# Performance work log

Measured on AMD Instinct MI355X. Metric: run time of the kernel, lower is better.

The kernel has to match this reference:

```python
import jax, jax.numpy as jnp
import numpy as np

N_NODES = 100000
N_EDGES = 1600000
N_GRAPHS = 64
IN_F = 128
H_F = 128
N_CLS = 10


def setup_inputs() -> dict:
    key = jax.random.key(0)
    ks = jax.random.split(key, 10)
    feat = jax.random.normal(ks[0], (N_NODES, IN_F), dtype=jnp.float32)
    W1 = jax.random.normal(ks[1], (IN_F, H_F), dtype=jnp.float32) * 0.05
    b1 = jax.random.normal(ks[2], (H_F,), dtype=jnp.float32) * 0.05
    W2 = jax.random.normal(ks[3], (H_F, H_F), dtype=jnp.float32) * 0.05
    b2 = jax.random.normal(ks[4], (H_F,), dtype=jnp.float32) * 0.05
    Wp = jax.random.normal(ks[5], (H_F, N_CLS), dtype=jnp.float32) * 0.05
    bp = jax.random.normal(ks[6], (N_CLS,), dtype=jnp.float32) * 0.05
    src = jax.random.randint(ks[7], (N_EDGES,), 0, N_NODES, dtype=jnp.int32)
    dst = jax.random.randint(ks[8], (N_EDGES,), 0, N_NODES, dtype=jnp.int32)
    graph_id = jnp.sort(jax.random.randint(ks[9], (N_NODES,), 0, N_GRAPHS, dtype=jnp.int32))
    return {"feat": feat, "W1": W1, "b1": b1, "W2": W2, "b2": b2,
            "Wp": Wp, "bp": bp, "src": src, "dst": dst, "graph_id": graph_id}


def reference(feat, W1, b1, W2, b2, Wp, bp, src, dst, graph_id):
    # copy_u + sum: each dst node sums features of its source neighbors
    def agg(h):
        return jax.ops.segment_sum(h[src], dst, num_segments=N_NODES)

    h = jax.nn.relu(agg(feat) @ W1 + b1)   # conv1 + ReLU
    h = jax.nn.relu(agg(h) @ W2 + b2)      # conv2 + ReLU (num_messagepasses=2)

    # dgl.mean_nodes: per-graph mean pooling over nodes
    sums = jax.ops.segment_sum(h, graph_id, num_segments=N_GRAPHS)      # [G, H]
    cnts = jax.ops.segment_sum(jnp.ones((N_NODES, 1), h.dtype), graph_id,
                               num_segments=N_GRAPHS)                    # [G, 1]
    graph_feats = sums / jnp.maximum(cnts, 1.0)
    return graph_feats @ Wp + bp
```

## Files before the change

kernel.cpp:

```cpp
#include <hip/hip_runtime.h>

#define NF 128
#define NGRAPHS 64
#define NCLS 10
#define NPARTS 256
#define PART_SHIFT 9
#define PART_NODES 512
#define PART_CAP 9216
#define SPLIT_TILE 2048
#define AS_STRIDE 136
#define SRC_BITS 17

typedef __attribute__((ext_vector_type(8))) short bf16x8;
typedef __attribute__((ext_vector_type(4))) float f32x4;
typedef __attribute__((ext_vector_type(8))) unsigned short u16x8;

__device__ __forceinline__ float bf2f(unsigned short u) {
    union { unsigned int i; float f; } v; v.i = ((unsigned int)u) << 16; return v.f;
}
__device__ __forceinline__ unsigned short f2bf(float f) {
    union { float f; unsigned int i; } v; v.f = f;
    unsigned int lsb = (v.i >> 16) & 1;
    v.i += 0x7fffu + lsb;
    return (unsigned short)(v.i >> 16);
}

__device__ __forceinline__ void gather_node(
    const unsigned short* __restrict__ x, const int* __restrict__ offs,
    const int* __restrict__ eid, int node, int n, int c, float acc[8]) {
#pragma unroll
    for (int r = 0; r < 8; ++r) acc[r] = 0.f;
    if (node >= n) return;
    int j = offs[node];
    int end = offs[node + 1];
    for (; j + 8 <= end; j += 8) {
        int s0 = eid[j + 0], s1 = eid[j + 1], s2 = eid[j + 2], s3 = eid[j + 3];
        int s4 = eid[j + 4], s5 = eid[j + 5], s6 = eid[j + 6], s7 = eid[j + 7];
        u16x8 v0 = ((const u16x8*)(x + (size_t)s0 * NF))[c];
        u16x8 v1 = ((const u16x8*)(x + (size_t)s1 * NF))[c];
        u16x8 v2 = ((const u16x8*)(x + (size_t)s2 * NF))[c];
        u16x8 v3 = ((const u16x8*)(x + (size_t)s3 * NF))[c];
        u16x8 v4 = ((const u16x8*)(x + (size_t)s4 * NF))[c];
        u16x8 v5 = ((const u16x8*)(x + (size_t)s5 * NF))[c];
        u16x8 v6 = ((const u16x8*)(x + (size_t)s6 * NF))[c];
        u16x8 v7 = ((const u16x8*)(x + (size_t)s7 * NF))[c];
#pragma unroll
        for (int r = 0; r < 8; ++r)
            acc[r] += ((bf2f(v0[r]) + bf2f(v1[r])) + (bf2f(v2[r]) + bf2f(v3[r])))
                    + ((bf2f(v4[r]) + bf2f(v5[r])) + (bf2f(v6[r]) + bf2f(v7[r])));
    }
    if (j + 4 <= end) {
        int s0 = eid[j + 0], s1 = eid[j + 1], s2 = eid[j + 2], s3 = eid[j + 3];
        u16x8 v0 = ((const u16x8*)(x + (size_t)s0 * NF))[c];
        u16x8 v1 = ((const u16x8*)(x + (size_t)s1 * NF))[c];
        u16x8 v2 = ((const u16x8*)(x + (size_t)s2 * NF))[c];
        u16x8 v3 = ((const u16x8*)(x + (size_t)s3 * NF))[c];
#pragma unroll
        for (int r = 0; r < 8; ++r)
            acc[r] += (bf2f(v0[r]) + bf2f(v1[r])) + (bf2f(v2[r]) + bf2f(v3[r]));
        j += 4;
    }
    for (; j < end; ++j) {
        int s0 = eid[j];
        u16x8 v0 = ((const u16x8*)(x + (size_t)s0 * NF))[c];
#pragma unroll
        for (int r = 0; r < 8; ++r) acc[r] += bf2f(v0[r]);
    }
}

__global__ __launch_bounds__(256) void prep_kernel(
    const float* __restrict__ feat, unsigned short* __restrict__ featbf,
    const float* __restrict__ W1, const float* __restrict__ W2,
    unsigned short* __restrict__ Wt1, unsigned short* __restrict__ Wt2,
    float* __restrict__ sums, int* __restrict__ gcur, int nv4) {
    int gtid = blockIdx.x * 256 + threadIdx.x;
    int nthreads = gridDim.x * 256;
    for (int i = gtid; i < nv4; i += nthreads) {
        float4 v = ((const float4*)feat)[i];
        ushort4 o;
        o.x = f2bf(v.x); o.y = f2bf(v.y); o.z = f2bf(v.z); o.w = f2bf(v.w);
        ((ushort4*)featbf)[i] = o;
    }
    for (int i = gtid; i < 2 * NF * NF; i += nthreads) {
        const float* W = (i < NF * NF) ? W1 : W2;
        unsigned short* Wt = (i < NF * NF) ? Wt1 : Wt2;
        int id = i & (NF * NF - 1);
        int f = id >> 7;
        int k = id & 127;
        Wt[f * NF + k] = f2bf(W[k * NF + f]);
    }
    for (int i = gtid; i < NGRAPHS * NF; i += nthreads) sums[i] = 0.f;
    if (gtid < NPARTS) gcur[gtid] = 0;
}

__global__ __launch_bounds__(256) void split_kernel(
    const int* __restrict__ src, const int* __restrict__ dst,
    unsigned int* __restrict__ records, int* __restrict__ gcur, int ne) {
    __shared__ unsigned int stage[SPLIT_TILE];
    __shared__ int hcnt[NPARTS];
    __shared__ int hscan[NPARTS];
    __shared__ int hcur[NPARTS];
    __shared__ int hg[NPARTS];
    int t = threadIdx.x;

    int tile0 = blockIdx.x * SPLIT_TILE;
    int cnt = min(SPLIT_TILE, ne - tile0);
    if (cnt <= 0) return;
    hcnt[t] = 0;
    __syncthreads();
    int dv[SPLIT_TILE / 256], sv[SPLIT_TILE / 256];
#pragma unroll
    for (int k2 = 0; k2 < SPLIT_TILE / 256; ++k2) {
        int i = k2 * 256 + t;
        if (i < cnt) {
            dv[k2] = dst[tile0 + i];
            sv[k2] = src[tile0 + i];
            atomicAdd(&hcnt[dv[k2] >> PART_SHIFT], 1);
        }
    }
    __syncthreads();
    hscan[t] = hcnt[t];
    __syncthreads();
    for (int off = 1; off < NPARTS; off <<= 1) {
        int v = (t >= off) ? hscan[t - off] : 0;
        __syncthreads();
        hscan[t] += v;
        __syncthreads();
    }
    hcur[t] = hscan[t] - hcnt[t];
    hg[t] = hcnt[t] ? atomicAdd(&gcur[t], hcnt[t]) : 0;
    __syncthreads();
#pragma unroll
    for (int k2 = 0; k2 < SPLIT_TILE / 256; ++k2) {
        int i = k2 * 256 + t;
        if (i < cnt) {
            int d = dv[k2];
            int pos = atomicAdd(&hcur[d >> PART_SHIFT], 1);
            stage[pos] = (((unsigned int)(d & (PART_NODES - 1))) << SRC_BITS)
                         | (unsigned int)sv[k2];
        }
    }
    __syncthreads();
    int grp = t >> 4;
    int lt = t & 15;
    for (int p = grp; p < NPARTS; p += 16) {
        int c = hcnt[p];
        if (c == 0) continue;
        int b = hscan[p] - c;
        int g = hg[p];
        if (g + c > PART_CAP) c = max(0, PART_CAP - g);
        unsigned int* outp = records + (size_t)p * PART_CAP + g;
        for (int i = lt; i < c; i += 16) outp[i] = stage[b + i];
    }
}

__global__ __launch_bounds__(256) void build_kernel(
    const unsigned int* __restrict__ records, const int* __restrict__ gcur,
    int* __restrict__ offs, int* __restrict__ eid, int n) {
    __shared__ int deg[PART_NODES];
    __shared__ int ps[NPARTS];
    __shared__ int wsum[4];
    __shared__ unsigned int rc[PART_CAP];
    int t = threadIdx.x;
    int p = blockIdx.x;

    ps[t] = min(gcur[t], PART_CAP);
    __syncthreads();
    for (int off = 1; off < NPARTS; off <<= 1) {
        int v = (t >= off) ? ps[t - off] : 0;
        __syncthreads();
        ps[t] += v;
        __syncthreads();
    }
    int L = min(gcur[p], PART_CAP);
    int base_g = ps[p] - L;
    if (p == 0 && t == 0) offs[n] = ps[NPARTS - 1];

    int lo = p << PART_SHIFT;
    int nn = min(n - lo, PART_NODES);
    if (nn <= 0) return;

    deg[t] = 0;
    deg[t + 256] = 0;
    __syncthreads();

    const unsigned int* rp = records + (size_t)p * PART_CAP;
    for (int i = t; i < L; i += 256) {
        unsigned int r = rp[i];
        rc[i] = r;
        atomicAdd(&deg[r >> SRC_BITS], 1);
    }
    __syncthreads();

    int v0 = deg[2 * t];
    int v1 = deg[2 * t + 1];
    int tsum = v0 + v1;
    int lane = t & 63, w = t >> 6;
    int sc = tsum;
    for (int off = 1; off < 64; off <<= 1) {
        int u = __shfl_up(sc, off, 64);
        if (lane >= off) sc += u;
    }
    if (lane == 63) wsum[w] = sc;
    __syncthreads();
    if (t == 0) {
        int a = 0;
        for (int k = 0; k < 4; ++k) { int v = wsum[k]; wsum[k] = a; a += v; }
    }
    __syncthreads();
    int run = sc - tsum + wsum[w];
    deg[2 * t] = run;
    if (2 * t < nn) offs[lo + 2 * t] = base_g + run;
    run += v0;
    deg[2 * t + 1] = run;
    if (2 * t + 1 < nn) offs[lo + 2 * t + 1] = base_g + run;
    __syncthreads();

    for (int i = t; i < L; i += 256) {
        unsigned int r = rc[i];
        int pos = atomicAdd(&deg[r >> SRC_BITS], 1);
        eid[base_g + pos] = (int)(r & ((1u << SRC_BITS) - 1));
    }
}

__global__ __launch_bounds__(256) void gather_gemm1(
    const unsigned short* __restrict__ x, const int* __restrict__ offs,
    const int* __restrict__ eid, const unsigned short* __restrict__ Wt,
    const float* __restrict__ bias, unsigned short* __restrict__ out, int n) {
    __shared__ unsigned short As[16 * AS_STRIDE];
    int wave = threadIdx.x >> 6;
    int lane = threadIdx.x & 63;
    int q = lane >> 4;
    int c = lane & 15;
    int node_base = blockIdx.x * 16;
    int row = wave * 4 + q;

    float acc[8];
    gather_node(x, offs, eid, node_base + row, n, c, acc);
    {
        u16x8 o;
#pragma unroll
        for (int r = 0; r < 8; ++r) o[r] = f2bf(acc[r]);
        *(u16x8*)(&As[row * AS_STRIDE + c * 8]) = o;
    }
    __syncthreads();

    int m16 = c;
    int n0 = wave * 32;
    const unsigned short* b0r = Wt + (size_t)(n0 + m16) * NF + q * 8;
    const unsigned short* b1r = b0r + 16 * NF;
    f32x4 acc0 = {0.f, 0.f, 0.f, 0.f};
    f32x4 acc1 = {0.f, 0.f, 0.f, 0.f};
#pragma unroll
    for (int kk = 0; kk < 4; ++kk) {
        bf16x8 a  = *(const bf16x8*)(&As[m16 * AS_STRIDE + kk * 32 + q * 8]);
        bf16x8 b0 = *(const bf16x8*)(b0r + kk * 32);
        bf16x8 b1 = *(const bf16x8*)(b1r + kk * 32);
        acc0 = __builtin_amdgcn_mfma_f32_16x16x32_bf16(a, b0, acc0, 0, 0, 0);
        acc1 = __builtin_amdgcn_mfma_f32_16x16x32_bf16(a, b1, acc1, 0, 0, 0);
    }
    float bias0 = bias[n0 + m16];
    float bias1 = bias[n0 + 16 + m16];
#pragma unroll
    for (int r = 0; r < 4; ++r) {
        int node = node_base + q * 4 + r;
        if (node >= n) break;
        unsigned short* o = out + (size_t)node * NF;
        o[n0 + m16]      = f2bf(fmaxf(acc0[r] + bias0, 0.f));
        o[n0 + 16 + m16] = f2bf(fmaxf(acc1[r] + bias1, 0.f));
    }
}

__global__ __launch_bounds__(256) void gather_gemm2_pool(
    const unsigned short* __restrict__ x, const int* __restrict__ offs,
    const int* __restrict__ eid, const unsigned short* __restrict__ Wt,
    const float* __restrict__ bias, const int* __restrict__ gid,
    float* __restrict__ sums, int n) {
    __shared__ unsigned short As[16 * AS_STRIDE];
    __shared__ float hblk[16][NF];
    int wave = threadIdx.x >> 6;
    int lane = threadIdx.x & 63;
    int q = lane >> 4;
    int c = lane & 15;
    int node_base = blockIdx.x * 16;
    int row = wave * 4 + q;

    float acc[8];
    gather_node(x, offs, eid, node_base + row, n, c, acc);
    {
        u16x8 o;
#pragma unroll
        for (int r = 0; r < 8; ++r) o[r] = f2bf(acc[r]);
        *(u16x8*)(&As[row * AS_STRIDE + c * 8]) = o;
    }
    __syncthreads();

    int m16 = c;
    int n0 = wave * 32;
    const unsigned short* b0r = Wt + (size_t)(n0 + m16) * NF + q * 8;
    const unsigned short* b1r = b0r + 16 * NF;
    f32x4 acc0 = {0.f, 0.f, 0.f, 0.f};
    f32x4 acc1 = {0.f, 0.f, 0.f, 0.f};
#pragma unroll
    for (int kk = 0; kk < 4; ++kk) {
        bf16x8 a  = *(const bf16x8*)(&As[m16 * AS_STRIDE + kk * 32 + q * 8]);
        bf16x8 b0 = *(const bf16x8*)(b0r + kk * 32);
        bf16x8 b1 = *(const bf16x8*)(b1r + kk * 32);
        acc0 = __builtin_amdgcn_mfma_f32_16x16x32_bf16(a, b0, acc0, 0, 0, 0);
        acc1 = __builtin_amdgcn_mfma_f32_16x16x32_bf16(a, b1, acc1, 0, 0, 0);
    }
    float bias0 = bias[n0 + m16];
    float bias1 = bias[n0 + 16 + m16];
#pragma unroll
    for (int r = 0; r < 4; ++r) {
        int rr = q * 4 + r;
        hblk[rr][n0 + m16]      = fmaxf(acc0[r] + bias0, 0.f);
        hblk[rr][n0 + 16 + m16] = fmaxf(acc1[r] + bias1, 0.f);
    }
    __syncthreads();

    int t = threadIdx.x;
    if (t < NF) {
        float accp = 0.f;
        int cur = -1;
        int lim = min(16, n - node_base);
        for (int i = 0; i < lim; ++i) {
            int g = gid[node_base + i];
            if (g != cur) {
                if (cur >= 0) atomicAdd(&sums[cur * NF + t], accp);
                accp = 0.f;
                cur = g;
            }
            accp += bf2f(f2bf(hblk[i][t]));
        }
        if (cur >= 0) atomicAdd(&sums[cur * NF + t], accp);
    }
}

__device__ __forceinline__ int lower_bound_i(const int* a, int n, int key) {
    int lo = 0, hi = n;
    while (lo < hi) {
        int mid = (lo + hi) >> 1;
        if (a[mid] < key) lo = mid + 1; else hi = mid;
    }
    return lo;
}

__global__ __launch_bounds__(64) void final_kernel(
    const float* __restrict__ sums, const int* __restrict__ gid, int n,
    const float* __restrict__ Wp, const float* __restrict__ bp,
    float* __restrict__ out) {
    __shared__ int range[2];
    int g = blockIdx.x;
    int lane = threadIdx.x;
    if (lane == 0) range[0] = lower_bound_i(gid, n, g);
    if (lane == 1) range[1] = lower_bound_i(gid, n, g + 1);
    __syncthreads();
    float cnt = fmaxf((float)(range[1] - range[0]), 1.0f);
    float inv = 1.0f / cnt;
    float s0 = sums[g * NF + lane] * inv;
    float s1 = sums[g * NF + 64 + lane] * inv;
#pragma unroll
    for (int c = 0; c < NCLS; ++c) {
        float p = s0 * Wp[lane * NCLS + c] + s1 * Wp[(64 + lane) * NCLS + c];
#pragma unroll
        for (int m = 1; m < 64; m <<= 1) p += __shfl_xor(p, m, 64);
        if (lane == 0) out[g * NCLS + c] = p + bp[c];
    }
}

extern "C" void kernel_launch(void* const* d_in, const int* in_sizes, int n_in,
                              void* d_out, int out_size, void* d_ws, size_t ws_size,
                              hipStream_t stream) {
    const float* feat = (const float*)d_in[0];
    const float* W1   = (const float*)d_in[1];
    const float* b1   = (const float*)d_in[2];
    const float* W2   = (const float*)d_in[3];
    const float* b2   = (const float*)d_in[4];
    const float* Wp   = (const float*)d_in[5];
    const float* bp   = (const float*)d_in[6];
    const int*   src  = (const int*)d_in[7];
    const int*   dst  = (const int*)d_in[8];
    const int*   gid  = (const int*)d_in[9];

    int ne = in_sizes[7];
    int n  = in_sizes[9];

    unsigned short* featbf = (unsigned short*)d_ws;
    unsigned short* h1     = featbf + (size_t)n * NF;
    unsigned int* records = (unsigned int*)(h1 + (size_t)n * NF);
    int* eid      = (int*)(records + (size_t)NPARTS * PART_CAP);
    float* sums   = (float*)(eid + ne);
    int* gcur     = (int*)(sums + NGRAPHS * NF);
    unsigned short* Wt1 = (unsigned short*)(gcur + NPARTS);
    unsigned short* Wt2 = Wt1 + NF * NF;
    int* offs     = (int*)(Wt2 + NF * NF);

    int nv4 = n * NF / 4;
    int splitblocks = (ne + SPLIT_TILE - 1) / SPLIT_TILE;
    int buildblocks = (n + PART_NODES - 1) >> PART_SHIFT;
    int ggblocks = (n + 15) / 16;

    prep_kernel<<<1024, 256, 0, stream>>>(
        feat, featbf, W1, W2, Wt1, Wt2, sums, gcur, nv4);
    split_kernel<<<splitblocks, 256, 0, stream>>>(src, dst, records, gcur, ne);
    build_kernel<<<buildblocks, 256, 0, stream>>>(records, gcur, offs, eid, n);

    gather_gemm1<<<ggblocks, 256, 0, stream>>>(featbf, offs, eid, Wt1, b1, h1, n);
    gather_gemm2_pool<<<ggblocks, 256, 0, stream>>>(h1, offs, eid, Wt2, b2, gid, sums, n);
    final_kernel<<<NGRAPHS, 64, 0, stream>>>(sums, gid, n, Wp, bp, (float*)d_out);
}
```

Before: 309.6 us.

## Replace partitioned CSR build with global degree count, single-block scan, atomic scatter

Replaces the two-pass partitioned bucketing (split into per-partition record buffers, then per-partition local sort) with a classic CSR build. Degrees are counted via global atomics inside the prep kernel, prefix-summed by a single 1024-thread block, and edges are scattered with per-node global atomic cursors. This removes the capped partition buffers and their possible truncation. In exchange it adds 1.6M scattered global atomics twice, a serial single-block scan over 100k nodes, and an extra memset. Neighbour order within each node also becomes nondeterministic, which may hurt gather locality.

```diff
diff --git a/kernel.cpp b/kernel.cpp
--- a/kernel.cpp
+++ b/kernel.cpp
@@ -3,13 +3,8 @@
 #define NF 128
 #define NGRAPHS 64
 #define NCLS 10
-#define NPARTS 256
-#define PART_SHIFT 9
-#define PART_NODES 512
-#define PART_CAP 9216
-#define SPLIT_TILE 2048
 #define AS_STRIDE 136
-#define SRC_BITS 17
+#define SCAN_THREADS 1024
 
 typedef __attribute__((ext_vector_type(8))) short bf16x8;
 typedef __attribute__((ext_vector_type(4))) float f32x4;
@@ -72,7 +67,8 @@
     const float* __restrict__ feat, unsigned short* __restrict__ featbf,
     const float* __restrict__ W1, const float* __restrict__ W2,
     unsigned short* __restrict__ Wt1, unsigned short* __restrict__ Wt2,
-    float* __restrict__ sums, int* __restrict__ gcur, int nv4) {
+    float* __restrict__ sums, const int* __restrict__ dst,
+    int* __restrict__ degree, int ne, int nv4) {
     int gtid = blockIdx.x * 256 + threadIdx.x;
     int nthreads = gridDim.x * 256;
     for (int i = gtid; i < nv4; i += nthreads) {
@@ -90,136 +86,68 @@
         Wt[f * NF + k] = f2bf(W[k * NF + f]);
     }
     for (int i = gtid; i < NGRAPHS * NF; i += nthreads) sums[i] = 0.f;
-    if (gtid < NPARTS) gcur[gtid] = 0;
-}
-
-__global__ __launch_bounds__(256) void split_kernel(
+    for (int i = gtid; i < ne; i += nthreads) {
+        atomicAdd(&degree[dst[i]], 1);
+    }
+}
+
+__global__ __launch_bounds__(SCAN_THREADS) void scan_kernel(
+    const int* __restrict__ deg, int* __restrict__ offs,
+    int* __restrict__ cursor, int n) {
+    __shared__ int wsums[16];
+    __shared__ int carry_s;
+    int t = threadIdx.x;
+    int lane = t & 63, w = t >> 6;
+    if (t == 0) carry_s = 0;
+    __syncthreads();
+    for (int base = 0; base < n; base += SCAN_THREADS * 4) {
+        int i0 = base + t * 4;
+        int v[4];
+#pragma unroll
+        for (int k = 0; k < 4; ++k) {
+            int i = i0 + k;
+            v[k] = (i < n) ? deg[i] : 0;
+        }
+        int tsum = v[0] + v[1] + v[2] + v[3];
+        int sc = tsum;
+        for (int off = 1; off < 64; off <<= 1) {
+            int u = __shfl_up(sc, off, 64);
+            if (lane >= off) sc += u;
+        }
+        if (lane == 63) wsums[w] = sc;
+        __syncthreads();
+        if (w == 0 && lane < 16) {
+            int x = wsums[lane];
+            for (int off = 1; off < 16; off <<= 1) {
+                int u = __shfl_up(x, off, 64);
+                if (lane >= off) x += u;
+            }
+            wsums[lane] = x;
+        }
+        __syncthreads();
+        int wbase = (w == 0) ? 0 : wsums[w - 1];
+        int excl = carry_s + wbase + (sc - tsum);
+#pragma unroll
+        for (int k = 0; k < 4; ++k) {
+            int i = i0 + k;
+            if (i < n) { offs[i] = excl; cursor[i] = excl; }
+            excl += v[k];
+        }
+        __syncthreads();
+        if (t == 0) carry_s += wsums[15];
+        __syncthreads();
+    }
+    if (t == 0) offs[n] = carry_s;
+}
+
+__global__ __launch_bounds__(256) void scatter_kernel(
     const int* __restrict__ src, const int* __restrict__ dst,
-    unsigned int* __restrict__ records, int* __restrict__ gcur, int ne) {
-    __shared__ unsigned int stage[SPLIT_TILE];
-    __shared__ int hcnt[NPARTS];
-    __shared__ int hscan[NPARTS];
-    __shared__ int hcur[NPARTS];
-    __shared__ int hg[NPARTS];
-    int t = threadIdx.x;
-
-    int tile0 = blockIdx.x * SPLIT_TILE;
-    int cnt = min(SPLIT_TILE, ne - tile0);
-    if (cnt <= 0) return;
-    hcnt[t] = 0;
-    __syncthreads();
-    int dv[SPLIT_TILE / 256], sv[SPLIT_TILE / 256];
-#pragma unroll
-    for (int k2 = 0; k2 < SPLIT_TILE / 256; ++k2) {
-        int i = k2 * 256 + t;
-        if (i < cnt) {
-            dv[k2] = dst[tile0 + i];
-            sv[k2] = src[tile0 + i];
-            atomicAdd(&hcnt[dv[k2] >> PART_SHIFT], 1);
-        }
-    }
-    __syncthreads();
-    hscan[t] = hcnt[t];
-    __syncthreads();
-    for (int off = 1; off < NPARTS; off <<= 1) {
-        int v = (t >= off) ? hscan[t - off] : 0;
-        __syncthreads();
-        hscan[t] += v;
-        __syncthreads();
-    }
-    hcur[t] = hscan[t] - hcnt[t];
-    hg[t] = hcnt[t] ? atomicAdd(&gcur[t], hcnt[t]) : 0;
-    __syncthreads();
-#pragma unroll
-    for (int k2 = 0; k2 < SPLIT_TILE / 256; ++k2) {
-        int i = k2 * 256 + t;
-        if (i < cnt) {
-            int d = dv[k2];
-            int pos = atomicAdd(&hcur[d >> PART_SHIFT], 1);
-            stage[pos] = (((unsigned int)(d & (PART_NODES - 1))) << SRC_BITS)
-                         | (unsigned int)sv[k2];
-        }
-    }
-    __syncthreads();
-    int grp = t >> 4;
-    int lt = t & 15;
-    for (int p = grp; p < NPARTS; p += 16) {
-        int c = hcnt[p];
-        if (c == 0) continue;
-        int b = hscan[p] - c;
-        int g = hg[p];
-        if (g + c > PART_CAP) c = max(0, PART_CAP - g);
-        unsigned int* outp = records + (size_t)p * PART_CAP + g;
-        for (int i = lt; i < c; i += 16) outp[i] = stage[b + i];
-    }
-}
-
-__global__ __launch_bounds__(256) void build_kernel(
-    const unsigned int* __restrict__ records, const int* __restrict__ gcur,
-    int* __restrict__ offs, int* __restrict__ eid, int n) {
-    __shared__ int deg[PART_NODES];
-    __shared__ int ps[NPARTS];
-    __shared__ int wsum[4];
-    __shared__ unsigned int rc[PART_CAP];
-    int t = threadIdx.x;
-    int p = blockIdx.x;
-
-    ps[t] = min(gcur[t], PART_CAP);
-    __syncthreads();
-    for (int off = 1; off < NPARTS; off <<= 1) {
-        int v = (t >= off) ? ps[t - off] : 0;
-        __syncthreads();
-        ps[t] += v;
-        __syncthreads();
-    }
-    int L = min(gcur[p], PART_CAP);
-    int base_g = ps[p] - L;
-    if (p == 0 && t == 0) offs[n] = ps[NPARTS - 1];
-
-    int lo = p << PART_SHIFT;
-    int nn = min(n - lo, PART_NODES);
-    if (nn <= 0) return;
-
-    deg[t] = 0;
-    deg[t + 256] = 0;
-    __syncthreads();
-
-    const unsigned int* rp = records + (size_t)p * PART_CAP;
-    for (int i = t; i < L; i += 256) {
-        unsigned int r = rp[i];
-        rc[i] = r;
-        atomicAdd(&deg[r >> SRC_BITS], 1);
-    }
-    __syncthreads();
-
-    int v0 = deg[2 * t];
-    int v1 = deg[2 * t + 1];
-    int tsum = v0 + v1;
-    int lane = t & 63, w = t >> 6;
-    int sc = tsum;
-    for (int off = 1; off < 64; off <<= 1) {
-        int u = __shfl_up(sc, off, 64);
-        if (lane >= off) sc += u;
-    }
-    if (lane == 63) wsum[w] = sc;
-    __syncthreads();
-    if (t == 0) {
-        int a = 0;
-        for (int k = 0; k < 4; ++k) { int v = wsum[k]; wsum[k] = a; a += v; }
-    }
-    __syncthreads();
-    int run = sc - tsum + wsum[w];
-    deg[2 * t] = run;
-    if (2 * t < nn) offs[lo + 2 * t] = base_g + run;
-    run += v0;
-    deg[2 * t + 1] = run;
-    if (2 * t + 1 < nn) offs[lo + 2 * t + 1] = base_g + run;
-    __syncthreads();
-
-    for (int i = t; i < L; i += 256) {
-        unsigned int r = rc[i];
-        int pos = atomicAdd(&deg[r >> SRC_BITS], 1);
-        eid[base_g + pos] = (int)(r & ((1u << SRC_BITS) - 1));
+    int* __restrict__ cursor, int* __restrict__ eid, int ne) {
+    int i = blockIdx.x * 256 + threadIdx.x;
+    if (i < ne) {
+        int d = dst[i];
+        int pos = atomicAdd(&cursor[d], 1);
+        eid[pos] = src[i];
     }
 }
 
@@ -388,23 +316,23 @@
 
     unsigned short* featbf = (unsigned short*)d_ws;
     unsigned short* h1     = featbf + (size_t)n * NF;
-    unsigned int* records = (unsigned int*)(h1 + (size_t)n * NF);
-    int* eid      = (int*)(records + (size_t)NPARTS * PART_CAP);
-    float* sums   = (float*)(eid + ne);
-    int* gcur     = (int*)(sums + NGRAPHS * NF);
-    unsigned short* Wt1 = (unsigned short*)(gcur + NPARTS);
+    int* eid      = (int*)(h1 + (size_t)n * NF);
+    int* degree   = eid + ne;
+    int* cursor   = degree + n;
+    int* offs     = cursor + n;
+    float* sums   = (float*)(offs + n + 4);
+    unsigned short* Wt1 = (unsigned short*)(sums + NGRAPHS * NF);
     unsigned short* Wt2 = Wt1 + NF * NF;
-    int* offs     = (int*)(Wt2 + NF * NF);
 
     int nv4 = n * NF / 4;
-    int splitblocks = (ne + SPLIT_TILE - 1) / SPLIT_TILE;
-    int buildblocks = (n + PART_NODES - 1) >> PART_SHIFT;
+    int scatterblocks = (ne + 255) / 256;
     int ggblocks = (n + 15) / 16;
 
+    hipMemsetAsync(degree, 0, (size_t)n * sizeof(int), stream);
     prep_kernel<<<1024, 256, 0, stream>>>(
-        feat, featbf, W1, W2, Wt1, Wt2, sums, gcur, nv4);
-    split_kernel<<<splitblocks, 256, 0, stream>>>(src, dst, records, gcur, ne);
-    build_kernel<<<buildblocks, 256, 0, stream>>>(records, gcur, offs, eid, n);
+        feat, featbf, W1, W2, Wt1, Wt2, sums, dst, degree, ne, nv4);
+    scan_kernel<<<1, SCAN_THREADS, 0, stream>>>(degree, offs, cursor, n);
+    scatter_kernel<<<scatterblocks, 256, 0, stream>>>(src, dst, cursor, eid, ne);
 
     gather_gemm1<<<ggblocks, 256, 0, stream>>>(featbf, offs, eid, Wt1, b1, h1, n);
     gather_gemm2_pool<<<ggblocks, 256, 0, stream>>>(h1, offs, eid, Wt2, b2, gid, sums, n);
```

Result: slower. 537.0 us (+73.5%).
